# Kernel tuning notes

Measured on AMD Instinct MI355X. Metric: run time of the kernel, lower is better.

The kernel has to match this reference:

```python
import jax, jax.numpy as jnp
import numpy as np

DT = 0.01
NJ = 7
GRAV = 9.81
Q_LOWER = jnp.array([-2.9671, -1.8326, -2.9671, -3.1416, -2.9671, -0.0873, -2.9671], jnp.float32)
Q_UPPER = jnp.array([ 2.9671,  1.8326,  2.9671,  0.0,     2.9671,  3.8223,  2.9671], jnp.float32)


def _skew(v):
    z = jnp.zeros((), v.dtype)
    return jnp.stack([jnp.stack([z, -v[2], v[1]]),
                      jnp.stack([v[2], z, -v[0]]),
                      jnp.stack([-v[1], v[0], z])])


def _mot_X(E, r):
    # 6x6 spatial motion transform [[E,0],[-E*skew(r),E]]
    zero = jnp.zeros_like(E)
    top = jnp.concatenate([E, zero], axis=1)
    bot = jnp.concatenate([-E @ _skew(r), E], axis=1)
    return jnp.concatenate([top, bot], axis=0)


def _crm(v):
    # spatial motion cross-product matrix for v=[w;v0]
    Sw, Sv = _skew(v[:3]), _skew(v[3:])
    zero = jnp.zeros_like(Sw)
    top = jnp.concatenate([Sw, zero], axis=1)
    bot = jnp.concatenate([Sv, Sw], axis=1)
    return jnp.concatenate([top, bot], axis=0)


def _step_single(x, u, axes, R_tree, p_tree, I_sp):
    dt_ = x.dtype
    q = jnp.clip(x[:NJ], Q_LOWER.astype(dt_), Q_UPPER.astype(dt_))
    qd = x[NJ:]
    # forward kinematics: per-joint 6x6 child<-parent transforms and motion subspaces
    Xups, Ss = [], []
    eye3 = jnp.eye(3, dtype=dt_)
    for i in range(NJ):
        a = axes[i]
        c, s = jnp.cos(q[i]), jnp.sin(q[i])
        R = c * eye3 + s * _skew(a) + (1.0 - c) * jnp.outer(a, a)  # rodrigues
        Xj = _mot_X(R.T, jnp.zeros(3, dt_))
        Xt = _mot_X(R_tree[i], p_tree[i])
        Xups.append(Xj @ Xt)
        Ss.append(jnp.concatenate([a, jnp.zeros(3, dt_)]))
    # RNEA bias force h (qdd=0, gravity, zero base velocity, identity base pose)
    v_prev = jnp.zeros(6, dt_)
    a_prev = jnp.array([0.0, 0.0, 0.0, 0.0, 0.0, GRAV], dt_)  # a_base = -g trick
    fs = []
    for i in range(NJ):
        vJ = Ss[i] * qd[i]
        v = Xups[i] @ v_prev + vJ
        acc = Xups[i] @ a_prev + _crm(v) @ vJ
        Iv = I_sp[i] @ v
        f = I_sp[i] @ acc - _crm(v).T @ Iv  # crf(v) = -crm(v)^T
        fs.append(f)
        v_prev, a_prev = v, acc
    h = [None] * NJ
    for i in range(NJ - 1, -1, -1):
        h[i] = Ss[i] @ fs[i]
        if i > 0:
            fs[i - 1] = fs[i - 1] + Xups[i].T @ fs[i]
    h = jnp.stack(h)
    # CRBA mass matrix (serial chain, parent(i)=i-1)
    Ic = [I_sp[i] for i in range(NJ)]
    M = jnp.zeros((NJ, NJ), dt_)
    for i in range(NJ - 1, -1, -1):
        if i > 0:
            Ic[i - 1] = Ic[i - 1] + Xups[i].T @ Ic[i] @ Xups[i]
        F = Ic[i] @ Ss[i]
        M = M.at[i, i].set(Ss[i] @ F)
        for j in range(i - 1, -1, -1):
            F = Xups[j + 1].T @ F
            mij = Ss[j] @ F
            M = M.at[i, j].set(mij).at[j, i].set(mij)
    M = M + 1e-8 * jnp.eye(NJ, dtype=dt_)
    qdd = jnp.linalg.solve(M, (u - h)[:, None])[:, 0]
    qd_new = qd + DT * qdd
    q_new = q + DT * qd_new
    return jnp.concatenate([q_new, qd_new])


def setup_inputs() -> dict:
    B = 65536
    key = jax.random.key(0)
    k1, k2 = jax.random.split(key)
    x = jax.random.normal(k1, (B, 14), jnp.float32)
    u = jax.random.normal(k2, (B, 7), jnp.float32)
    rng = np.random.default_rng(0)
    # unit joint axes
    axes = rng.normal(size=(NJ, 3))
    axes = axes / np.linalg.norm(axes, axis=1, keepdims=True)
    # orthonormal fixed parent->child rotations (det +1)
    R_tree = np.empty((NJ, 3, 3))
    for i in range(NJ):
        Q, _ = np.linalg.qr(rng.normal(size=(3, 3)))
        if np.linalg.det(Q) < 0:
            Q[:, 0] = -Q[:, 0]
        R_tree[i] = Q
    p_tree = 0.2 * rng.normal(size=(NJ, 3))
    # SPD 6x6 spatial inertias: [[Ibar, m*Cx],[m*Cx^T, m*I3]]
    I_sp = np.empty((NJ, 6, 6))
    for i in range(NJ):
        m = float(rng.uniform(1.0, 5.0))
        c = 0.05 * rng.normal(size=3)
        Cx = np.array([[0, -c[2], c[1]], [c[2], 0, -c[0]], [-c[1], c[0], 0]])
        A = 0.1 * rng.normal(size=(3, 3))
        Ic_ = A @ A.T + 0.05 * np.eye(3)
        Ibar = Ic_ + m * Cx @ Cx.T
        I_sp[i] = np.block([[Ibar, m * Cx], [m * Cx.T, m * np.eye(3)]])
    return {
        "x": x, "u": u,
        "axes": jnp.asarray(axes, jnp.float32),
        "R_tree": jnp.asarray(R_tree, jnp.float32),
        "p_tree": jnp.asarray(p_tree, jnp.float32),
        "I_sp": jnp.asarray(I_sp, jnp.float32),
    }


def reference(x, u, axes, R_tree, p_tree, I_sp):
    return jax.vmap(_step_single, in_axes=(0, 0, None, None, None, None))(
        x, u, axes, R_tree, p_tree, I_sp)
```

## Files before the change

kernel.cpp:

```cpp
#include <hip/hip_runtime.h>
#include <math.h>

#define NJ 7
#define DTF 0.01f
#define GRAVF 9.81f
#define MIX(i,j) ((i)*((i)+1)/2 + (j))
#define MPAD 29

__device__ __forceinline__ void cross3(const float* a, const float* b, float* o){
    o[0] = a[1]*b[2] - a[2]*b[1];
    o[1] = a[2]*b[0] - a[0]*b[2];
    o[2] = a[0]*b[1] - a[1]*b[0];
}
__device__ __forceinline__ void mv3(const float* E, const float* x, float* y){
    y[0] = E[0]*x[0] + E[1]*x[1] + E[2]*x[2];
    y[1] = E[3]*x[0] + E[4]*x[1] + E[5]*x[2];
    y[2] = E[6]*x[0] + E[7]*x[1] + E[8]*x[2];
}
__device__ __forceinline__ void mtv3(const float* E, const float* x, float* y){
    y[0] = E[0]*x[0] + E[3]*x[1] + E[6]*x[2];
    y[1] = E[1]*x[0] + E[4]*x[1] + E[7]*x[2];
    y[2] = E[2]*x[0] + E[5]*x[1] + E[8]*x[2];
}
__device__ __forceinline__ void symv(const float* S, const float* x, float* y){
    y[0] = S[0]*x[0] + S[1]*x[1] + S[2]*x[2];
    y[1] = S[1]*x[0] + S[3]*x[1] + S[4]*x[2];
    y[2] = S[2]*x[0] + S[4]*x[1] + S[5]*x[2];
}
__device__ __forceinline__ void mm3(const float* A, const float* B, float* o){
#pragma unroll
    for (int r = 0; r < 3; r++)
#pragma unroll
        for (int c = 0; c < 3; c++)
            o[r*3+c] = A[r*3]*B[c] + A[r*3+1]*B[3+c] + A[r*3+2]*B[6+c];
}
__device__ __forceinline__ void congr(const float* E, const float* X, float* o){
    float t[9];
#pragma unroll
    for (int r = 0; r < 3; r++)
#pragma unroll
        for (int c = 0; c < 3; c++)
            t[r*3+c] = E[r]*X[c] + E[3+r]*X[3+c] + E[6+r]*X[6+c];
    mm3(t, E, o);
}
__device__ __forceinline__ void makeE(const float* a, const float* __restrict__ Rt,
                                      float s, float c, float* E){
    float omc = 1.0f - c;
    float RT[9];
    RT[0] = c + omc*a[0]*a[0];       RT[1] =  s*a[2] + omc*a[0]*a[1]; RT[2] = -s*a[1] + omc*a[0]*a[2];
    RT[3] = -s*a[2] + omc*a[1]*a[0]; RT[4] = c + omc*a[1]*a[1];       RT[5] =  s*a[0] + omc*a[1]*a[2];
    RT[6] =  s*a[1] + omc*a[2]*a[0]; RT[7] = -s*a[0] + omc*a[2]*a[1]; RT[8] = c + omc*a[2]*a[2];
    float Rl[9];
#pragma unroll
    for (int k = 0; k < 9; k++) Rl[k] = Rt[k];
    mm3(RT, Rl, E);
}
__device__ __forceinline__ void bodyI(const float* __restrict__ g_I, int i,
                                      float* SA, float* h, float& m){
    const float* I6 = g_I + i*36;
    SA[0]=I6[0]; SA[1]=I6[1]; SA[2]=I6[2];
    SA[3]=I6[7]; SA[4]=I6[8]; SA[5]=I6[14];
    h[0]=I6[16]; h[1]=I6[5]; h[2]=I6[9];
    m = I6[21];
}
__device__ __forceinline__ void congrBase(const float* Ec, const float* rc,
                                          const float* SA, const float* h, float m,
                                          float* SA0, float* h0){
    float Af[9] = {SA[0],SA[1],SA[2], SA[1],SA[3],SA[4], SA[2],SA[4],SA[5]};
    float Ap[9]; congr(Ec, Af, Ap);
    float hr[3]; mtv3(Ec, h, hr);
    float hpd = hr[0]*rc[0]+hr[1]*rc[1]+hr[2]*rc[2];
    float ppd = rc[0]*rc[0]+rc[1]*rc[1]+rc[2]*rc[2];
    float dga = 2.0f*hpd + m*ppd;
    SA0[0] = Ap[0] - 2.0f*rc[0]*hr[0] - m*rc[0]*rc[0] + dga;
    SA0[1] = Ap[1] - rc[0]*hr[1] - hr[0]*rc[1] - m*rc[0]*rc[1];
    SA0[2] = Ap[2] - rc[0]*hr[2] - hr[0]*rc[2] - m*rc[0]*rc[2];
    SA0[3] = Ap[4] - 2.0f*rc[1]*hr[1] - m*rc[1]*rc[1] + dga;
    SA0[4] = Ap[5] - rc[1]*hr[2] - hr[1]*rc[2] - m*rc[1]*rc[2];
    SA0[5] = Ap[8] - 2.0f*rc[2]*hr[2] - m*rc[2]*rc[2] + dga;
    h0[0] = hr[0] + m*rc[0];
    h0[1] = hr[1] + m*rc[1];
    h0[2] = hr[2] + m*rc[2];
}

__constant__ float QL_c[NJ] = {-2.9671f,-1.8326f,-2.9671f,-3.1416f,-2.9671f,-0.0873f,-2.9671f};
__constant__ float QU_c[NJ] = { 2.9671f, 1.8326f, 2.9671f, 0.0f,    2.9671f, 3.8223f, 2.9671f};

__global__ __launch_bounds__(128)
void panda_step(const float* __restrict__ x, const float* __restrict__ u,
                const float* __restrict__ g_ax, const float* __restrict__ g_Rt,
                const float* __restrict__ g_pt, const float* __restrict__ g_I,
                float* __restrict__ out, int B)
{
    __shared__ float s_M[64*MPAD];

    const int role = threadIdx.x >> 6;
    const int lane = threadIdx.x & 63;
    const int e    = blockIdx.x*64 + lane;
    const bool act = (e < B);

    float q[NJ], qd[NJ], sn[NJ], cs[NJ];
    if (act){
        float xl[14];
        const float2* x2 = (const float2*)(x + e*14);
#pragma unroll
        for (int i = 0; i < 7; i++){ float2 v = x2[i]; xl[2*i] = v.x; xl[2*i+1] = v.y; }
#pragma unroll
        for (int i = 0; i < NJ; i++){
            q[i]  = fminf(fmaxf(xl[i], QL_c[i]), QU_c[i]);
            qd[i] = xl[NJ + i];
            __sincosf(q[i], &sn[i], &cs[i]);
        }
    }

    float rhs[NJ];

    if (act && role == 1){
        float Sw[NJ][3], Sv[NJ][3];
        float SB[NJ][6], hB[NJ][3];
        float Ec[9], rc[3];
#pragma unroll
        for (int i = 0; i < NJ; i++){
            float a[3] = { g_ax[3*i], g_ax[3*i+1], g_ax[3*i+2] };
            float p[3] = { g_pt[3*i], g_pt[3*i+1], g_pt[3*i+2] };
            float E[9]; makeE(a, g_Rt + 9*i, sn[i], cs[i], E);
            if (i == 0){
#pragma unroll
                for (int k = 0; k < 9; k++) Ec[k] = E[k];
                rc[0]=p[0]; rc[1]=p[1]; rc[2]=p[2];
            } else {
                float t3[3]; mtv3(Ec, p, t3);
                rc[0]+=t3[0]; rc[1]+=t3[1]; rc[2]+=t3[2];
                float En[9]; mm3(E, Ec, En);
#pragma unroll
                for (int k = 0; k < 9; k++) Ec[k] = En[k];
            }
            float sh[3]; mtv3(Ec, a, sh);
            float cb[3]; cross3(rc, sh, cb);
#pragma unroll
            for (int k = 0; k < 3; k++){ Sw[i][k]=sh[k]; Sv[i][k]=cb[k]; }
            float SAb[6], hb[3], mb; bodyI(g_I, i, SAb, hb, mb);
            congrBase(Ec, rc, SAb, hb, mb, &SB[i][0], &hB[i][0]);
        }
        float IcA[6] = {0,0,0,0,0,0}, Ich[3] = {0,0,0}, Icm = 0.f;
        float Mx[28];
#pragma unroll
        for (int i = NJ-1; i >= 0; i--){
#pragma unroll
            for (int k = 0; k < 6; k++) IcA[k] += SB[i][k];
#pragma unroll
            for (int k = 0; k < 3; k++) Ich[k] += hB[i][k];
            Icm += g_I[i*36 + 21];
            float Ft[3], Fb[3], t1[3], t2[3];
            symv(IcA, &Sw[i][0], Ft);
            cross3(Ich, &Sv[i][0], t1);
#pragma unroll
            for (int k = 0; k < 3; k++) Ft[k] += t1[k];
            cross3(Ich, &Sw[i][0], t2);
#pragma unroll
            for (int k = 0; k < 3; k++) Fb[k] = Icm*Sv[i][k] - t2[k];
#pragma unroll
            for (int j = 0; j < NJ; j++) if (j <= i){
                Mx[MIX(i,j)] = Sw[j][0]*Ft[0] + Sw[j][1]*Ft[1] + Sw[j][2]*Ft[2]
                             + Sv[j][0]*Fb[0] + Sv[j][1]*Fb[1] + Sv[j][2]*Fb[2];
            }
        }
#pragma unroll
        for (int i = 0; i < NJ; i++) Mx[MIX(i,i)] += 1e-8f;
#pragma unroll
        for (int k = 0; k < NJ; k++){
            float d = Mx[MIX(k,k)];
#pragma unroll
            for (int j = 0; j < NJ; j++) if (j < k) d -= Mx[MIX(k,j)]*Mx[MIX(k,j)];
            float linv = __builtin_amdgcn_rsqf(d);
            Mx[MIX(k,k)] = linv;
#pragma unroll
            for (int i2 = k+1; i2 < NJ; i2++){
                float s2 = Mx[MIX(i2,k)];
#pragma unroll
                for (int j = 0; j < NJ; j++) if (j < k) s2 -= Mx[MIX(i2,j)]*Mx[MIX(k,j)];
                Mx[MIX(i2,k)] = s2 * linv;
            }
        }
#pragma unroll
        for (int j = 0; j < 28; j++) s_M[lane*MPAD + j] = Mx[j];
    }
    else if (act){
#pragma unroll
        for (int i = 0; i < NJ; i++) rhs[i] = u[e*NJ + i];
        float Earr[NJ][9];
        float FF[NJ][6];
        float w[3]  = {0.f,0.f,0.f}, vl[3] = {0.f,0.f,0.f};
        float aw[3] = {0.f,0.f,0.f}, av[3] = {0.f,0.f,GRAVF};
#pragma unroll
        for (int i = 0; i < NJ; i++){
            float a[3] = { g_ax[3*i], g_ax[3*i+1], g_ax[3*i+2] };
            float p[3] = { g_pt[3*i], g_pt[3*i+1], g_pt[3*i+2] };
            float* E = &Earr[i][0];
            makeE(a, g_Rt + 9*i, sn[i], cs[i], E);
            float qdi = qd[i];
            float tw[3]; mv3(E, w, tw);
            float nw[3] = { tw[0]+a[0]*qdi, tw[1]+a[1]*qdi, tw[2]+a[2]*qdi };
            float cwp[3]; cross3(w, p, cwp);
            float t1[3] = { vl[0]+cwp[0], vl[1]+cwp[1], vl[2]+cwp[2] };
            float nvl[3]; mv3(E, t1, nvl);
            float taw[3]; mv3(E, aw, taw);
            float cna[3]; cross3(nw, a, cna);
            float naw[3] = { taw[0]+qdi*cna[0], taw[1]+qdi*cna[1], taw[2]+qdi*cna[2] };
            float cap[3]; cross3(aw, p, cap);
            float t2[3] = { av[0]+cap[0], av[1]+cap[1], av[2]+cap[2] };
            float tav[3]; mv3(E, t2, tav);
            float cva[3]; cross3(nvl, a, cva);
            float nav[3] = { tav[0]+qdi*cva[0], tav[1]+qdi*cva[1], tav[2]+qdi*cva[2] };
            float SAi[6], hi[3], mi; bodyI(g_I, i, SAi, hi, mi);
            float Ivt[3], Iat[3], hxv[3], hxa[3];
            symv(SAi, nw, Ivt);  cross3(hi, nvl, hxv);
            symv(SAi, naw, Iat); cross3(hi, nav, hxa);
#pragma unroll
            for (int k = 0; k < 3; k++){ Ivt[k] += hxv[k]; Iat[k] += hxa[k]; }
            float hxw[3], hxaw[3];
            cross3(hi, nw, hxw); cross3(hi, naw, hxaw);
            float Ivb[3] = { mi*nvl[0]-hxw[0], mi*nvl[1]-hxw[1], mi*nvl[2]-hxw[2] };
            float Iab[3] = { mi*nav[0]-hxaw[0], mi*nav[1]-hxaw[1], mi*nav[2]-hxaw[2] };
            float c1[3], c2[3], c3[3];
            cross3(nw, Ivt, c1); cross3(nvl, Ivb, c2); cross3(nw, Ivb, c3);
            FF[i][0] = Iat[0]+c1[0]+c2[0];
            FF[i][1] = Iat[1]+c1[1]+c2[1];
            FF[i][2] = Iat[2]+c1[2]+c2[2];
            FF[i][3] = Iab[0]+c3[0];
            FF[i][4] = Iab[1]+c3[1];
            FF[i][5] = Iab[2]+c3[2];
#pragma unroll
            for (int k = 0; k < 3; k++){ w[k]=nw[k]; vl[k]=nvl[k]; aw[k]=naw[k]; av[k]=nav[k]; }
        }
#pragma unroll
        for (int i = NJ-1; i >= 0; i--){
            float a[3] = { g_ax[3*i], g_ax[3*i+1], g_ax[3*i+2] };
            rhs[i] -= a[0]*FF[i][0] + a[1]*FF[i][1] + a[2]*FF[i][2];
            if (i > 0){
                float p[3] = { g_pt[3*i], g_pt[3*i+1], g_pt[3*i+2] };
                const float* E = &Earr[i][0];
                float tm[3], tf[3], cp[3];
                mtv3(E, &FF[i][0], tm); mtv3(E, &FF[i][3], tf);
                cross3(p, tf, cp);
                FF[i-1][0]+=tm[0]+cp[0]; FF[i-1][1]+=tm[1]+cp[1]; FF[i-1][2]+=tm[2]+cp[2];
                FF[i-1][3]+=tf[0];       FF[i-1][4]+=tf[1];       FF[i-1][5]+=tf[2];
            }
        }
    }

    __syncthreads();

    if (act && role == 0){
        float Mx[28];
#pragma unroll
        for (int j = 0; j < 28; j++) Mx[j] = s_M[lane*MPAD + j];
        float y[NJ];
#pragma unroll
        for (int i = 0; i < NJ; i++){
            float s2 = rhs[i];
#pragma unroll
            for (int j = 0; j < NJ; j++) if (j < i) s2 -= Mx[MIX(i,j)]*y[j];
            y[i] = s2 * Mx[MIX(i,i)];
        }
        float z[NJ];
#pragma unroll
        for (int i = NJ-1; i >= 0; i--){
            float s2 = y[i];
#pragma unroll
            for (int j = NJ-1; j >= 0; j--) if (j > i) s2 -= Mx[MIX(j,i)]*z[j];
            z[i] = s2 * Mx[MIX(i,i)];
        }
        float o14[14];
#pragma unroll
        for (int i = 0; i < NJ; i++){
            float qdn = qd[i] + DTF*z[i];
            o14[i]      = q[i] + DTF*qdn;
            o14[NJ + i] = qdn;
        }
        float2* o2 = (float2*)(out + e*14);
#pragma unroll
        for (int i = 0; i < 7; i++){ float2 v; v.x = o14[2*i]; v.y = o14[2*i+1]; o2[i] = v; }
    }
}

extern "C" void kernel_launch(void* const* d_in, const int* in_sizes, int n_in,
                              void* d_out, int out_size, void* d_ws, size_t ws_size,
                              hipStream_t stream) {
    const float* x   = (const float*)d_in[0];
    const float* u   = (const float*)d_in[1];
    const float* ax  = (const float*)d_in[2];
    const float* Rt  = (const float*)d_in[3];
    const float* pt  = (const float*)d_in[4];
    const float* Isp = (const float*)d_in[5];
    float* out = (float*)d_out;
    int B = in_sizes[0] / 14;
    int grid = (B + 63) / 64;
    hipLaunchKernelGGL(panda_step, dim3(grid), dim3(128), 0, stream,
                       x, u, ax, Rt, pt, Isp, out, B);
}
```

Before: 77.72 us.

## Rewrite CRBA as local-frame backward sweep and spill per-thread arrays to LDS

Replaces the base-frame CRBA (accumulating world transforms and congruences per body) with a local-frame recursion. It propagates the composite inertia child-to-parent and transports force columns joint by joint, with the columns kept in shared memory. Sin/cos, joint velocities and rhs are computed once by role 0 and shared through LDS, and the register arrays (Earr, FF) move to LDS with loops no longer unrolled. The aim is lower register pressure and higher occupancy, at the cost of an extra block barrier, more LDS traffic and recomputing E in the backward pass.

```diff
diff --git a/kernel.cpp b/kernel.cpp
--- a/kernel.cpp
+++ b/kernel.cpp
@@ -6,6 +6,9 @@
 #define GRAVF 9.81f
 #define MIX(i,j) ((i)*((i)+1)/2 + (j))
 #define MPAD 29
+#define FSTR 43
+#define SNC  15
+#define QST  9
 
 __device__ __forceinline__ void cross3(const float* a, const float* b, float* o){
     o[0] = a[1]*b[2] - a[2]*b[1];
@@ -63,25 +66,6 @@
     h[0]=I6[16]; h[1]=I6[5]; h[2]=I6[9];
     m = I6[21];
 }
-__device__ __forceinline__ void congrBase(const float* Ec, const float* rc,
-                                          const float* SA, const float* h, float m,
-                                          float* SA0, float* h0){
-    float Af[9] = {SA[0],SA[1],SA[2], SA[1],SA[3],SA[4], SA[2],SA[4],SA[5]};
-    float Ap[9]; congr(Ec, Af, Ap);
-    float hr[3]; mtv3(Ec, h, hr);
-    float hpd = hr[0]*rc[0]+hr[1]*rc[1]+hr[2]*rc[2];
-    float ppd = rc[0]*rc[0]+rc[1]*rc[1]+rc[2]*rc[2];
-    float dga = 2.0f*hpd + m*ppd;
-    SA0[0] = Ap[0] - 2.0f*rc[0]*hr[0] - m*rc[0]*rc[0] + dga;
-    SA0[1] = Ap[1] - rc[0]*hr[1] - hr[0]*rc[1] - m*rc[0]*rc[1];
-    SA0[2] = Ap[2] - rc[0]*hr[2] - hr[0]*rc[2] - m*rc[0]*rc[2];
-    SA0[3] = Ap[4] - 2.0f*rc[1]*hr[1] - m*rc[1]*rc[1] + dga;
-    SA0[4] = Ap[5] - rc[1]*hr[2] - hr[1]*rc[2] - m*rc[1]*rc[2];
-    SA0[5] = Ap[8] - 2.0f*rc[2]*hr[2] - m*rc[2]*rc[2] + dga;
-    h0[0] = hr[0] + m*rc[0];
-    h0[1] = hr[1] + m*rc[1];
-    h0[2] = hr[2] + m*rc[2];
-}
 
 __constant__ float QL_c[NJ] = {-2.9671f,-1.8326f,-2.9671f,-3.1416f,-2.9671f,-0.0873f,-2.9671f};
 __constant__ float QU_c[NJ] = { 2.9671f, 1.8326f, 2.9671f, 0.0f,    2.9671f, 3.8223f, 2.9671f};
@@ -93,14 +77,18 @@
                 float* __restrict__ out, int B)
 {
     __shared__ float s_M[64*MPAD];
+    __shared__ float s_F[2*64*FSTR];
+    __shared__ float s_snc[64*SNC];
+    __shared__ float s_qd[64*QST];
+    __shared__ float s_rhs[64*QST];
 
     const int role = threadIdx.x >> 6;
     const int lane = threadIdx.x & 63;
     const int e    = blockIdx.x*64 + lane;
     const bool act = (e < B);
 
-    float q[NJ], qd[NJ], sn[NJ], cs[NJ];
-    if (act){
+    float q[NJ], qd[NJ];
+    if (act && role == 0){
         float xl[14];
         const float2* x2 = (const float2*)(x + e*14);
 #pragma unroll
@@ -109,62 +97,69 @@
         for (int i = 0; i < NJ; i++){
             q[i]  = fminf(fmaxf(xl[i], QL_c[i]), QU_c[i]);
             qd[i] = xl[NJ + i];
-            __sincosf(q[i], &sn[i], &cs[i]);
+            float s, c; __sincosf(q[i], &s, &c);
+            s_snc[lane*SNC + i]     = s;
+            s_snc[lane*SNC + 7 + i] = c;
+            s_qd[lane*QST + i]      = qd[i];
+            s_rhs[lane*QST + i]     = u[e*NJ + i];
         }
     }
-
-    float rhs[NJ];
+    __syncthreads();
 
     if (act && role == 1){
-        float Sw[NJ][3], Sv[NJ][3];
-        float SB[NJ][6], hB[NJ][3];
-        float Ec[9], rc[3];
-#pragma unroll
-        for (int i = 0; i < NJ; i++){
+        float* Fb = &s_F[64*FSTR + lane*FSTR];
+        float SA[6], hc[3], mc;
+        bodyI(g_I, 6, SA, hc, mc);
+#pragma unroll 1
+        for (int i = NJ-1; i >= 0; --i){
             float a[3] = { g_ax[3*i], g_ax[3*i+1], g_ax[3*i+2] };
             float p[3] = { g_pt[3*i], g_pt[3*i+1], g_pt[3*i+2] };
-            float E[9]; makeE(a, g_Rt + 9*i, sn[i], cs[i], E);
-            if (i == 0){
-#pragma unroll
-                for (int k = 0; k < 9; k++) Ec[k] = E[k];
-                rc[0]=p[0]; rc[1]=p[1]; rc[2]=p[2];
-            } else {
-                float t3[3]; mtv3(Ec, p, t3);
-                rc[0]+=t3[0]; rc[1]+=t3[1]; rc[2]+=t3[2];
-                float En[9]; mm3(E, Ec, En);
-#pragma unroll
-                for (int k = 0; k < 9; k++) Ec[k] = En[k];
+            float Ft[3]; symv(SA, a, Ft);
+            Fb[i*6+0]=Ft[0]; Fb[i*6+1]=Ft[1]; Fb[i*6+2]=Ft[2];
+            Fb[i*6+3] = a[1]*hc[2] - a[2]*hc[1];
+            Fb[i*6+4] = a[2]*hc[0] - a[0]*hc[2];
+            Fb[i*6+5] = a[0]*hc[1] - a[1]*hc[0];
+#pragma unroll 1
+            for (int k = i; k < NJ; ++k){
+                float f0=Fb[k*6], f1=Fb[k*6+1], f2=Fb[k*6+2];
+                s_M[lane*MPAD + k*(k+1)/2 + i] = a[0]*f0 + a[1]*f1 + a[2]*f2;
             }
-            float sh[3]; mtv3(Ec, a, sh);
-            float cb[3]; cross3(rc, sh, cb);
-#pragma unroll
-            for (int k = 0; k < 3; k++){ Sw[i][k]=sh[k]; Sv[i][k]=cb[k]; }
-            float SAb[6], hb[3], mb; bodyI(g_I, i, SAb, hb, mb);
-            congrBase(Ec, rc, SAb, hb, mb, &SB[i][0], &hB[i][0]);
-        }
-        float IcA[6] = {0,0,0,0,0,0}, Ich[3] = {0,0,0}, Icm = 0.f;
+            if (i > 0){
+                float snv = s_snc[lane*SNC+i], csv = s_snc[lane*SNC+7+i];
+                float E[9]; makeE(a, g_Rt + 9*i, snv, csv, E);
+                float SAm[6], hm[3], mm_;
+                bodyI(g_I, i-1, SAm, hm, mm_);
+                float Af[9] = {SA[0],SA[1],SA[2], SA[1],SA[3],SA[4], SA[2],SA[4],SA[5]};
+                float Ap[9]; congr(E, Af, Ap);
+                float hr[3]; mtv3(E, hc, hr);
+                float hpd = hr[0]*p[0]+hr[1]*p[1]+hr[2]*p[2];
+                float ppd = p[0]*p[0]+p[1]*p[1]+p[2]*p[2];
+                float dga = 2.0f*hpd + mc*ppd;
+                SA[0] = Ap[0] - 2.0f*p[0]*hr[0] - mc*p[0]*p[0] + dga + SAm[0];
+                SA[1] = Ap[1] - p[0]*hr[1] - hr[0]*p[1] - mc*p[0]*p[1] + SAm[1];
+                SA[2] = Ap[2] - p[0]*hr[2] - hr[0]*p[2] - mc*p[0]*p[2] + SAm[2];
+                SA[3] = Ap[4] - 2.0f*p[1]*hr[1] - mc*p[1]*p[1] + dga + SAm[3];
+                SA[4] = Ap[5] - p[1]*hr[2] - hr[1]*p[2] - mc*p[1]*p[2] + SAm[4];
+                SA[5] = Ap[8] - 2.0f*p[2]*hr[2] - mc*p[2]*p[2] + dga + SAm[5];
+                hc[0] = hr[0] + mc*p[0] + hm[0];
+                hc[1] = hr[1] + mc*p[1] + hm[1];
+                hc[2] = hr[2] + mc*p[2] + hm[2];
+                mc += mm_;
+#pragma unroll 1
+                for (int k = i; k < NJ; ++k){
+                    float ft[3] = {Fb[k*6+0], Fb[k*6+1], Fb[k*6+2]};
+                    float fb[3] = {Fb[k*6+3], Fb[k*6+4], Fb[k*6+5]};
+                    float tm[3], tf[3], cp[3];
+                    mtv3(E, ft, tm); mtv3(E, fb, tf);
+                    cross3(p, tf, cp);
+                    Fb[k*6+0]=tm[0]+cp[0]; Fb[k*6+1]=tm[1]+cp[1]; Fb[k*6+2]=tm[2]+cp[2];
+                    Fb[k*6+3]=tf[0];       Fb[k*6+4]=tf[1];       Fb[k*6+5]=tf[2];
+                }
+            }
+        }
         float Mx[28];
 #pragma unroll
-        for (int i = NJ-1; i >= 0; i--){
-#pragma unroll
-            for (int k = 0; k < 6; k++) IcA[k] += SB[i][k];
-#pragma unroll
-            for (int k = 0; k < 3; k++) Ich[k] += hB[i][k];
-            Icm += g_I[i*36 + 21];
-            float Ft[3], Fb[3], t1[3], t2[3];
-            symv(IcA, &Sw[i][0], Ft);
-            cross3(Ich, &Sv[i][0], t1);
-#pragma unroll
-            for (int k = 0; k < 3; k++) Ft[k] += t1[k];
-            cross3(Ich, &Sw[i][0], t2);
-#pragma unroll
-            for (int k = 0; k < 3; k++) Fb[k] = Icm*Sv[i][k] - t2[k];
-#pragma unroll
-            for (int j = 0; j < NJ; j++) if (j <= i){
-                Mx[MIX(i,j)] = Sw[j][0]*Ft[0] + Sw[j][1]*Ft[1] + Sw[j][2]*Ft[2]
-                             + Sv[j][0]*Fb[0] + Sv[j][1]*Fb[1] + Sv[j][2]*Fb[2];
-            }
-        }
+        for (int j = 0; j < 28; j++) Mx[j] = s_M[lane*MPAD + j];
 #pragma unroll
         for (int i = 0; i < NJ; i++) Mx[MIX(i,i)] += 1e-8f;
 #pragma unroll
@@ -186,19 +181,16 @@
         for (int j = 0; j < 28; j++) s_M[lane*MPAD + j] = Mx[j];
     }
     else if (act){
-#pragma unroll
-        for (int i = 0; i < NJ; i++) rhs[i] = u[e*NJ + i];
-        float Earr[NJ][9];
-        float FF[NJ][6];
+        float* Fb = &s_F[lane*FSTR];
         float w[3]  = {0.f,0.f,0.f}, vl[3] = {0.f,0.f,0.f};
         float aw[3] = {0.f,0.f,0.f}, av[3] = {0.f,0.f,GRAVF};
-#pragma unroll
-        for (int i = 0; i < NJ; i++){
+#pragma unroll 1
+        for (int i = 0; i < NJ; ++i){
             float a[3] = { g_ax[3*i], g_ax[3*i+1], g_ax[3*i+2] };
             float p[3] = { g_pt[3*i], g_pt[3*i+1], g_pt[3*i+2] };
-            float* E = &Earr[i][0];
-            makeE(a, g_Rt + 9*i, sn[i], cs[i], E);
-            float qdi = qd[i];
+            float snv = s_snc[lane*SNC+i], csv = s_snc[lane*SNC+7+i];
+            float qdi = s_qd[lane*QST+i];
+            float E[9]; makeE(a, g_Rt + 9*i, snv, csv, E);
             float tw[3]; mv3(E, w, tw);
             float nw[3] = { tw[0]+a[0]*qdi, tw[1]+a[1]*qdi, tw[2]+a[2]*qdi };
             float cwp[3]; cross3(w, p, cwp);
@@ -224,27 +216,35 @@
             float Iab[3] = { mi*nav[0]-hxaw[0], mi*nav[1]-hxaw[1], mi*nav[2]-hxaw[2] };
             float c1[3], c2[3], c3[3];
             cross3(nw, Ivt, c1); cross3(nvl, Ivb, c2); cross3(nw, Ivb, c3);
-            FF[i][0] = Iat[0]+c1[0]+c2[0];
-            FF[i][1] = Iat[1]+c1[1]+c2[1];
-            FF[i][2] = Iat[2]+c1[2]+c2[2];
-            FF[i][3] = Iab[0]+c3[0];
-            FF[i][4] = Iab[1]+c3[1];
-            FF[i][5] = Iab[2]+c3[2];
+            Fb[i*6+0] = Iat[0]+c1[0]+c2[0];
+            Fb[i*6+1] = Iat[1]+c1[1]+c2[1];
+            Fb[i*6+2] = Iat[2]+c1[2]+c2[2];
+            Fb[i*6+3] = Iab[0]+c3[0];
+            Fb[i*6+4] = Iab[1]+c3[1];
+            Fb[i*6+5] = Iab[2]+c3[2];
 #pragma unroll
             for (int k = 0; k < 3; k++){ w[k]=nw[k]; vl[k]=nvl[k]; aw[k]=naw[k]; av[k]=nav[k]; }
         }
-#pragma unroll
-        for (int i = NJ-1; i >= 0; i--){
+#pragma unroll 1
+        for (int i = NJ-1; i >= 0; --i){
             float a[3] = { g_ax[3*i], g_ax[3*i+1], g_ax[3*i+2] };
-            rhs[i] -= a[0]*FF[i][0] + a[1]*FF[i][1] + a[2]*FF[i][2];
+            float f0=Fb[i*6+0], f1=Fb[i*6+1], f2=Fb[i*6+2];
+            s_rhs[lane*QST+i] -= a[0]*f0 + a[1]*f1 + a[2]*f2;
             if (i > 0){
                 float p[3] = { g_pt[3*i], g_pt[3*i+1], g_pt[3*i+2] };
-                const float* E = &Earr[i][0];
+                float snv = s_snc[lane*SNC+i], csv = s_snc[lane*SNC+7+i];
+                float E[9]; makeE(a, g_Rt + 9*i, snv, csv, E);
+                float ftop[3] = {f0, f1, f2};
+                float fbot[3] = {Fb[i*6+3], Fb[i*6+4], Fb[i*6+5]};
                 float tm[3], tf[3], cp[3];
-                mtv3(E, &FF[i][0], tm); mtv3(E, &FF[i][3], tf);
+                mtv3(E, ftop, tm); mtv3(E, fbot, tf);
                 cross3(p, tf, cp);
-                FF[i-1][0]+=tm[0]+cp[0]; FF[i-1][1]+=tm[1]+cp[1]; FF[i-1][2]+=tm[2]+cp[2];
-                FF[i-1][3]+=tf[0];       FF[i-1][4]+=tf[1];       FF[i-1][5]+=tf[2];
+                Fb[(i-1)*6+0] += tm[0]+cp[0];
+                Fb[(i-1)*6+1] += tm[1]+cp[1];
+                Fb[(i-1)*6+2] += tm[2]+cp[2];
+                Fb[(i-1)*6+3] += tf[0];
+                Fb[(i-1)*6+4] += tf[1];
+                Fb[(i-1)*6+5] += tf[2];
             }
         }
     }
@@ -255,6 +255,9 @@
         float Mx[28];
 #pragma unroll
         for (int j = 0; j < 28; j++) Mx[j] = s_M[lane*MPAD + j];
+        float rhs[NJ];
+#pragma unroll
+        for (int i = 0; i < NJ; i++) rhs[i] = s_rhs[lane*QST + i];
         float y[NJ];
 #pragma unroll
         for (int i = 0; i < NJ; i++){
```

Result: no change. 77.28 us (-0.6%).
